# Kernel optimization log

Measured on AMD Instinct MI355X. Metric: run time of the kernel, lower is better.

Reference implementation:

```python
import jax, jax.numpy as jnp
import numpy as np

N = 50000      # nodes
E = 1200000    # edges (before self loops)
IN = 128       # in_channels
HID = 32       # hidden_channels
HEADS = 2
HC = HID * HEADS  # 64, per-layer output channels
OUT = 40       # classes
NEG_SLOPE = 0.2
BN_EPS = 1e-5


def setup_inputs() -> dict:
    key = jax.random.key(0)
    ks = jax.random.split(key, 20)
    def nrm(k, shape, scale=0.1):
        return jax.random.normal(k, shape, dtype=jnp.float32) * scale
    return {
        "x": jax.random.normal(ks[0], (N, IN), dtype=jnp.float32),
        "edge_index": jax.random.randint(ks[1], (2, E), 0, N),
        "W1": nrm(ks[2], (IN, HC)),
        "a_src1": nrm(ks[3], (HEADS, HID)),
        "a_dst1": nrm(ks[4], (HEADS, HID)),
        "b1": nrm(ks[5], (HC,)),
        "bn_gamma": 1.0 + nrm(ks[6], (HC,)),
        "bn_beta": nrm(ks[7], (HC,)),
        "bn_mean": nrm(ks[8], (HC,)),
        "bn_var": jax.random.uniform(ks[9], (HC,), minval=0.5, maxval=1.5),
        "W2": nrm(ks[10], (HC, HC)),
        "a_src2": nrm(ks[11], (HEADS, HID)),
        "a_dst2": nrm(ks[12], (HEADS, HID)),
        "b2": nrm(ks[13], (HC,)),
        "Wf": nrm(ks[14], (HC, OUT)),
        "bf": nrm(ks[15], (OUT,)),
    }


def _gat_conv(x, src, dst, W, a_s, a_d, b):
    # x: [N, F_in] -> h: [N, H, C]
    h = (x @ W).reshape(N, HEADS, HID)
    alpha_src = jnp.einsum("nhc,hc->nh", h, a_s)  # [N, H]
    alpha_dst = jnp.einsum("nhc,hc->nh", h, a_d)  # [N, H]
    e = alpha_src[src] + alpha_dst[dst]            # [E, H]
    e = jnp.where(e > 0, e, NEG_SLOPE * e)         # leaky_relu(0.2)
    # scatter softmax over edges grouped by dst node
    m = jax.ops.segment_max(e, dst, num_segments=N)
    m = jnp.where(jnp.isfinite(m), m, 0.0)         # isolated nodes -> -inf fill
    ee = jnp.exp(e - m[dst])
    denom = jax.ops.segment_sum(ee, dst, num_segments=N)
    alpha = ee / (denom[dst] + 1e-16)              # [E, H]
    # gather src features, weight by attention, scatter-add to dst
    out = jax.ops.segment_sum(h[src] * alpha[:, :, None], dst, num_segments=N)
    return out.reshape(N, HC) + b                  # concat heads + bias


def reference(x, edge_index, W1, a_src1, a_dst1, b1, bn_gamma, bn_beta,
              bn_mean, bn_var, W2, a_src2, a_dst2, b2, Wf, bf):
    # PyG GATConv adds self loops by default
    loop = jnp.arange(N, dtype=edge_index.dtype)
    src = jnp.concatenate([edge_index[0], loop])
    dst = jnp.concatenate([edge_index[1], loop])

    x1 = _gat_conv(x, src, dst, W1, a_src1, a_dst1, b1)
    x1 = (x1 - bn_mean) / jnp.sqrt(bn_var + BN_EPS) * bn_gamma + bn_beta  # BN eval
    x1 = jax.nn.elu(x1)
    # dropout is identity in eval mode
    x2 = _gat_conv(x1, src, dst, W2, a_src2, a_dst2, b2)
    jk = jnp.maximum(x1, x2)  # JumpingKnowledge 'max'
    logits = jk @ Wf + bf
    return jax.nn.log_softmax(logits, axis=1)
```

## Files before the change

kernel.cpp:

```cpp
#include <hip/hip_runtime.h>
#include <hip/hip_bf16.h>
#include <math.h>

#define N_NODES 50000
#define E_EDGES 1200000
#define E_TOT   (E_EDGES + N_NODES)
#define NEG_SLOPE 0.2f
#define BN_EPS 1e-5f
#define P_PART 196
#define B1 256
#define NSCAN (P_PART * B1)

__device__ __forceinline__ int rl_i(int v, int l) {
    return __builtin_amdgcn_readlane(v, l);
}
__device__ __forceinline__ float rl_f(float v, int l) {
    return __uint_as_float(__builtin_amdgcn_readlane(__float_as_uint(v), l));
}

__global__ void hist_kernel(const int* __restrict__ edst, unsigned* __restrict__ Ghist) {
    __shared__ unsigned hist[P_PART];
    for (int i = threadIdx.x; i < P_PART; i += 256) hist[i] = 0;
    __syncthreads();
    const int chunk = (E_TOT + B1 - 1) / B1;
    const int beg = blockIdx.x * chunk;
    const int end = min(beg + chunk, E_TOT);
    for (int i = beg + threadIdx.x; i < end; i += 256) {
        int d = (i < E_EDGES) ? edst[i] : (i - E_EDGES);
        atomicAdd(&hist[d >> 8], 1u);
    }
    __syncthreads();
    for (int p = threadIdx.x; p < P_PART; p += 256)
        Ghist[p * B1 + blockIdx.x] = hist[p];
}

__global__ void scan2_kernel(const unsigned* __restrict__ Ghist, unsigned* __restrict__ Goff) {
    __shared__ unsigned lds[1024];
    const int t = threadIdx.x;
    const int C = (NSCAN + 1023) / 1024;
    const int beg = t * C;
    const int end = min(beg + C, NSCAN);
    unsigned sum = 0;
    for (int i = beg; i < end; ++i) sum += Ghist[i];
    lds[t] = sum;
    __syncthreads();
    for (int off = 1; off < 1024; off <<= 1) {
        unsigned x = (t >= off) ? lds[t - off] : 0;
        __syncthreads();
        lds[t] += x;
        __syncthreads();
    }
    unsigned run = (t == 0) ? 0 : lds[t - 1];
    for (int i = beg; i < end; ++i) { Goff[i] = run; run += Ghist[i]; }
}

__global__ void partbase_kernel(const unsigned* __restrict__ Goff,
                                int* __restrict__ partbase, int* __restrict__ ptr) {
    int p = threadIdx.x;
    if (p < P_PART) partbase[p] = (int)Goff[p * B1];
    if (p == P_PART) partbase[P_PART] = E_TOT;
    if (p == 0) ptr[N_NODES] = E_TOT;
}

__global__ void scat2_kernel(const int* __restrict__ esrc, const int* __restrict__ edst,
                             const unsigned* __restrict__ Goff, unsigned* __restrict__ Gpart) {
    __shared__ unsigned cur[P_PART];
    for (int p = threadIdx.x; p < P_PART; p += 256) cur[p] = Goff[p * B1 + blockIdx.x];
    __syncthreads();
    const int chunk = (E_TOT + B1 - 1) / B1;
    const int beg = blockIdx.x * chunk;
    const int end = min(beg + chunk, E_TOT);
    for (int i = beg + threadIdx.x; i < end; i += 256) {
        int s = (i < E_EDGES) ? esrc[i] : (i - E_EDGES);
        int d = (i < E_EDGES) ? edst[i] : (i - E_EDGES);
        unsigned slot = atomicAdd(&cur[d >> 8], 1u);
        Gpart[slot] = ((unsigned)(d & 255) << 16) | (unsigned)s;
    }
}

__global__ void csr_kernel(const int* __restrict__ partbase, const unsigned* __restrict__ Gpart,
                           int* __restrict__ ptr, unsigned short* __restrict__ csr) {
    __shared__ unsigned deg[256];
    __shared__ unsigned scn[256];
    const int p = blockIdx.x;
    const int t = threadIdx.x;
    const int base = partbase[p];
    const int cnt = partbase[p + 1] - base;
    deg[t] = 0;
    __syncthreads();
    for (int i = t; i < cnt; i += 256)
        atomicAdd(&deg[Gpart[base + i] >> 16], 1u);
    __syncthreads();
    unsigned v = deg[t];
    scn[t] = v;
    __syncthreads();
    for (int o = 1; o < 256; o <<= 1) {
        unsigned x = (t >= o) ? scn[t - o] : 0;
        __syncthreads();
        scn[t] += x;
        __syncthreads();
    }
    unsigned excl = scn[t] - v;
    int node = p * 256 + t;
    if (node < N_NODES) ptr[node] = base + (int)excl;
    __syncthreads();
    deg[t] = excl;
    __syncthreads();
    for (int i = t; i < cnt; i += 256) {
        unsigned rec = Gpart[base + i];
        unsigned slot = atomicAdd(&deg[rec >> 16], 1u);
        csr[base + slot] = (unsigned short)(rec & 0xFFFFu);
    }
}

template<int K>
__global__ void lin_att_kernel(const float* __restrict__ x,
                               const float* __restrict__ W,
                               const float* __restrict__ a_s,
                               const float* __restrict__ a_d,
                               __hip_bfloat16* __restrict__ h,
                               float* __restrict__ asrc,
                               float* __restrict__ adst,
                               int n) {
    __shared__ float sW[K * 64];
    const int tid = threadIdx.x, lane = tid & 63;
    for (int i = tid; i < K * 64; i += 256) sW[i] = W[i];
    __syncthreads();
    const float a_sv = a_s[lane];
    const float a_dv = a_d[lane];
    const int wid = blockIdx.x * 4 + (tid >> 6);
    const int nwaves = gridDim.x * 4;
    for (int node = wid; node < n; node += nwaves) {
        float xr[K / 64];
        #pragma unroll
        for (int p = 0; p < K / 64; ++p) xr[p] = x[node * K + p * 64 + lane];
        float acc = 0.f;
        #pragma unroll
        for (int p = 0; p < K / 64; ++p) {
            #pragma unroll
            for (int k = 0; k < 64; ++k) {
                float xk = rl_f(xr[p], k);
                acc = fmaf(xk, sW[(p * 64 + k) * 64 + lane], acc);
            }
        }
        h[node * 64 + lane] = __float2bfloat16(acc);
        float ps = acc * a_sv, pd = acc * a_dv;
        #pragma unroll
        for (int m = 1; m < 32; m <<= 1) {
            ps += __shfl_xor(ps, m, 64);
            pd += __shfl_xor(pd, m, 64);
        }
        if ((lane & 31) == 0) {
            asrc[node * 2 + (lane >> 5)] = ps;
            adst[node * 2 + (lane >> 5)] = pd;
        }
    }
}

template<bool BN, bool FINAL>
__global__ void gat_agg_kernel(const int* __restrict__ ptr,
                               const unsigned short* __restrict__ csr_src,
                               const __hip_bfloat16* __restrict__ h,
                               const float2* __restrict__ asrc, const float2* __restrict__ adst,
                               const float* __restrict__ bias,
                               const float* __restrict__ gamma, const float* __restrict__ beta,
                               const float* __restrict__ mean, const float* __restrict__ var,
                               float* __restrict__ out,
                               const float* __restrict__ x1, const float* __restrict__ Wf,
                               const float* __restrict__ bf, float* __restrict__ out40) {
    __shared__ float sWf[FINAL ? 64 * 40 : 1];
    if constexpr (FINAL) {
        for (int i = threadIdx.x; i < 64 * 40; i += 256) sWf[i] = Wf[i];
        __syncthreads();
    }
    int node = blockIdx.x * 4 + (threadIdx.x >> 6);
    if (node >= N_NODES) return;
    const int lane = threadIdx.x & 63;
    const int half = lane & 31;
    float2 ad = adst[node];
    const float adh = (lane < 32) ? ad.x : ad.y;
    float m = -INFINITY, s = 0.f, acc = 0.f;
    const int beg = ptr[node], end = ptr[node + 1];
    for (int base = beg; base < end; base += 32) {
        const int cnt = min(32, end - base);
        int src = 0; float ev = -INFINITY;
        if (half < cnt) {
            src = (int)csr_src[base + half];
            float2 a2 = asrc[src];
            ev = ((lane < 32) ? a2.x : a2.y) + adh;
            ev = ev > 0.f ? ev : NEG_SLOPE * ev;
        }
        float cmax = ev;
        #pragma unroll
        for (int o = 1; o < 32; o <<= 1) cmax = fmaxf(cmax, __shfl_xor(cmax, o, 64));
        const float mn = fmaxf(m, cmax);
        const float rescale = __expf(m - mn);
        const float w = (half < cnt) ? __expf(ev - mn) : 0.f;
        float ws = w;
        #pragma unroll
        for (int o = 1; o < 32; o <<= 1) ws += __shfl_xor(ws, o, 64);
        s = s * rescale + ws;
        acc *= rescale;
        m = mn;
        int j = 0;
        for (; j + 4 <= cnt; j += 4) {
            int s0 = rl_i(src, j);
            int s1 = rl_i(src, j + 1);
            int s2 = rl_i(src, j + 2);
            int s3 = rl_i(src, j + 3);
            float wa0 = rl_f(w, j),      wb0 = rl_f(w, j + 32);
            float wa1 = rl_f(w, j + 1),  wb1 = rl_f(w, j + 33);
            float wa2 = rl_f(w, j + 2),  wb2 = rl_f(w, j + 34);
            float wa3 = rl_f(w, j + 3),  wb3 = rl_f(w, j + 35);
            float w0 = (lane < 32) ? wa0 : wb0;
            float w1 = (lane < 32) ? wa1 : wb1;
            float w2 = (lane < 32) ? wa2 : wb2;
            float w3 = (lane < 32) ? wa3 : wb3;
            float h0 = __bfloat162float(h[s0 * 64 + lane]);
            float h1 = __bfloat162float(h[s1 * 64 + lane]);
            float h2 = __bfloat162float(h[s2 * 64 + lane]);
            float h3 = __bfloat162float(h[s3 * 64 + lane]);
            acc = fmaf(w0, h0, acc);
            acc = fmaf(w1, h1, acc);
            acc = fmaf(w2, h2, acc);
            acc = fmaf(w3, h3, acc);
        }
        for (; j < cnt; ++j) {
            int sj = rl_i(src, j);
            float wa = rl_f(w, j), wb = rl_f(w, j + 32);
            float wj = (lane < 32) ? wa : wb;
            acc = fmaf(wj, __bfloat162float(h[sj * 64 + lane]), acc);
        }
    }
    float v = acc / (s + 1e-16f) + bias[lane];
    if constexpr (BN) {
        v = (v - mean[lane]) * rsqrtf(var[lane] + BN_EPS) * gamma[lane] + beta[lane];
        v = v > 0.f ? v : (__expf(v) - 1.f);
    }
    if constexpr (FINAL) {
        float jk = fmaxf(x1[node * 64 + lane], v);
        const int o = (lane < 40) ? lane : 0;
        float dot = 0.f;
        #pragma unroll
        for (int c = 0; c < 64; ++c) {
            float jv = rl_f(jk, c);
            dot = fmaf(jv, sWf[c * 40 + o], dot);
        }
        float logit = (lane < 40) ? (dot + bf[o]) : -INFINITY;
        float mx = logit;
        #pragma unroll
        for (int mm = 1; mm < 64; mm <<= 1) mx = fmaxf(mx, __shfl_xor(mx, mm, 64));
        float ex = (lane < 40) ? __expf(logit - mx) : 0.f;
        float sum = ex;
        #pragma unroll
        for (int mm = 1; mm < 64; mm <<= 1) sum += __shfl_xor(sum, mm, 64);
        if (lane < 40) out40[node * 40 + lane] = logit - mx - logf(sum);
    } else {
        out[node * 64 + lane] = v;
    }
}

extern "C" void kernel_launch(void* const* d_in, const int* in_sizes, int n_in,
                              void* d_out, int out_size, void* d_ws, size_t ws_size,
                              hipStream_t stream) {
    const float* x     = (const float*)d_in[0];
    const int*   ei    = (const int*)d_in[1];
    const float* W1    = (const float*)d_in[2];
    const float* as1   = (const float*)d_in[3];
    const float* ad1   = (const float*)d_in[4];
    const float* b1    = (const float*)d_in[5];
    const float* gamma = (const float*)d_in[6];
    const float* beta  = (const float*)d_in[7];
    const float* mean  = (const float*)d_in[8];
    const float* var   = (const float*)d_in[9];
    const float* W2    = (const float*)d_in[10];
    const float* as2   = (const float*)d_in[11];
    const float* ad2   = (const float*)d_in[12];
    const float* b2    = (const float*)d_in[13];
    const float* Wf    = (const float*)d_in[14];
    const float* bf    = (const float*)d_in[15];
    float* out = (float*)d_out;
    const int* esrc = ei;
    const int* edst = ei + E_EDGES;

    char* ws = (char*)d_ws;
    size_t off = 0;
    auto alloc = [&](size_t bytes) {
        char* p = ws + off;
        off += (bytes + 255) & ~(size_t)255;
        return p;
    };
    unsigned* Ghist = (unsigned*)alloc((size_t)NSCAN * 4);
    unsigned* Goff  = (unsigned*)alloc((size_t)NSCAN * 4);
    int* partbase   = (int*)alloc((size_t)(P_PART + 1) * 4);
    unsigned* Gpart = (unsigned*)alloc((size_t)E_TOT * 4);
    int* ptr             = (int*)alloc((size_t)(N_NODES + 1) * 4);
    unsigned short* csr  = (unsigned short*)alloc((size_t)E_TOT * 2);
    __hip_bfloat16* hbuf = (__hip_bfloat16*)alloc((size_t)N_NODES * 64 * 2);
    float* x1buf = (float*)alloc((size_t)N_NODES * 64 * 4);
    float* asrc  = (float*)alloc((size_t)N_NODES * 2 * 4);
    float* adst  = (float*)alloc((size_t)N_NODES * 2 * 4);
    (void)ws_size; (void)in_sizes; (void)n_in; (void)out_size;

    const int NB = (N_NODES + 3) / 4;

    hist_kernel<<<B1, 256, 0, stream>>>(edst, Ghist);
    scan2_kernel<<<1, 1024, 0, stream>>>(Ghist, Goff);
    partbase_kernel<<<1, 256, 0, stream>>>(Goff, partbase, ptr);
    scat2_kernel<<<B1, 256, 0, stream>>>(esrc, edst, Goff, Gpart);
    csr_kernel<<<P_PART, 256, 0, stream>>>(partbase, Gpart, ptr, csr);

    lin_att_kernel<128><<<2048, 256, 0, stream>>>(x, W1, as1, ad1, hbuf, asrc, adst, N_NODES);
    gat_agg_kernel<true, false><<<NB, 256, 0, stream>>>(ptr, csr, hbuf,
        (const float2*)asrc, (const float2*)adst,
        b1, gamma, beta, mean, var, x1buf, nullptr, nullptr, nullptr, nullptr);

    lin_att_kernel<64><<<2048, 256, 0, stream>>>(x1buf, W2, as2, ad2, hbuf, asrc, adst, N_NODES);
    gat_agg_kernel<false, true><<<NB, 256, 0, stream>>>(ptr, csr, hbuf,
        (const float2*)asrc, (const float2*)adst,
        b2, nullptr, nullptr, nullptr, nullptr, nullptr, x1buf, Wf, bf, out);
}
```

Baseline: 256.0 us.

## Precompute unnormalized edge attention weights and denominators in a separate per-partition kernel

```diff
diff --git a/kernel.cpp b/kernel.cpp
--- a/kernel.cpp
+++ b/kernel.cpp
@@ -16,6 +16,10 @@
 }
 __device__ __forceinline__ float rl_f(float v, int l) {
     return __uint_as_float(__builtin_amdgcn_readlane(__float_as_uint(v), l));
+}
+__device__ __forceinline__ unsigned bf16_bits(float f) {
+    unsigned u = __float_as_uint(f);
+    return (u + 0x7FFFu + ((u >> 16) & 1u)) >> 16;
 }
 
 __global__ void hist_kernel(const int* __restrict__ edst, unsigned* __restrict__ Ghist) {
@@ -79,7 +83,8 @@
 }
 
 __global__ void csr_kernel(const int* __restrict__ partbase, const unsigned* __restrict__ Gpart,
-                           int* __restrict__ ptr, unsigned short* __restrict__ csr) {
+                           int* __restrict__ ptr, unsigned short* __restrict__ csr,
+                           unsigned short* __restrict__ dl16) {
     __shared__ unsigned deg[256];
     __shared__ unsigned scn[256];
     const int p = blockIdx.x;
@@ -108,8 +113,47 @@
     __syncthreads();
     for (int i = t; i < cnt; i += 256) {
         unsigned rec = Gpart[base + i];
-        unsigned slot = atomicAdd(&deg[rec >> 16], 1u);
-        csr[base + slot] = (unsigned short)(rec & 0xFFFFu);
+        unsigned dl = rec >> 16;
+        unsigned slot = atomicAdd(&deg[dl], 1u);
+        csr[base + slot]  = (unsigned short)(rec & 0xFFFFu);
+        dl16[base + slot] = (unsigned short)dl;
+    }
+}
+
+__global__ void ew_kernel(const int* __restrict__ partbase,
+                          const unsigned short* __restrict__ csr,
+                          const unsigned short* __restrict__ dl16,
+                          const float2* __restrict__ asrc,
+                          const float2* __restrict__ adst,
+                          uint2* __restrict__ wrec,
+                          float2* __restrict__ denom) {
+    __shared__ float2 sad[256];
+    __shared__ float sden[512];
+    const int p = blockIdx.x, t = threadIdx.x;
+    if (t < 256) {
+        int node = p * 256 + t;
+        sad[t] = (node < N_NODES) ? adst[node] : make_float2(0.f, 0.f);
+    }
+    if (t < 512) sden[t] = 0.f;
+    __syncthreads();
+    const int base = partbase[p];
+    const int cnt = partbase[p + 1] - base;
+    for (int i = t; i < cnt; i += 1024) {
+        int s  = (int)csr[base + i];
+        int dl = (int)dl16[base + i];
+        float2 a = asrc[s];
+        float2 b = sad[dl];
+        float e0 = a.x + b.x; e0 = e0 > 0.f ? e0 : NEG_SLOPE * e0;
+        float e1 = a.y + b.y; e1 = e1 > 0.f ? e1 : NEG_SLOPE * e1;
+        float w0 = __expf(e0), w1 = __expf(e1);
+        atomicAdd(&sden[dl * 2 + 0], w0);
+        atomicAdd(&sden[dl * 2 + 1], w1);
+        wrec[base + i] = make_uint2((unsigned)s | (bf16_bits(w0) << 16), bf16_bits(w1));
+    }
+    __syncthreads();
+    if (t < 256) {
+        int node = p * 256 + t;
+        if (node < N_NODES) denom[node] = make_float2(sden[t * 2], sden[t * 2 + 1]);
     }
 }
 
@@ -159,9 +203,9 @@
 
 template<bool BN, bool FINAL>
 __global__ void gat_agg_kernel(const int* __restrict__ ptr,
-                               const unsigned short* __restrict__ csr_src,
+                               const uint2* __restrict__ wrec,
+                               const float2* __restrict__ denom,
                                const __hip_bfloat16* __restrict__ h,
-                               const float2* __restrict__ asrc, const float2* __restrict__ adst,
                                const float* __restrict__ bias,
                                const float* __restrict__ gamma, const float* __restrict__ beta,
                                const float* __restrict__ mean, const float* __restrict__ var,
@@ -177,62 +221,33 @@
     if (node >= N_NODES) return;
     const int lane = threadIdx.x & 63;
     const int half = lane & 31;
-    float2 ad = adst[node];
-    const float adh = (lane < 32) ? ad.x : ad.y;
-    float m = -INFINITY, s = 0.f, acc = 0.f;
+    const bool lo = (lane < 32);
+    float2 dn = denom[node];
+    const float den = lo ? dn.x : dn.y;
+    float acc = 0.f;
     const int beg = ptr[node], end = ptr[node + 1];
+
+#define EDGE(J) {                                                            \
+        unsigned rx = (unsigned)rl_i((int)rec.x, (J));                       \
+        unsigned ry = (unsigned)rl_i((int)rec.y, (J));                       \
+        const __hip_bfloat16* hp = h + (size_t)(rx & 0xFFFFu) * 64u;         \
+        float wv = __uint_as_float(lo ? (rx & 0xFFFF0000u) : (ry << 16));    \
+        acc = fmaf(wv, __bfloat162float(hp[lane]), acc); }
+
     for (int base = beg; base < end; base += 32) {
         const int cnt = min(32, end - base);
-        int src = 0; float ev = -INFINITY;
-        if (half < cnt) {
-            src = (int)csr_src[base + half];
-            float2 a2 = asrc[src];
-            ev = ((lane < 32) ? a2.x : a2.y) + adh;
-            ev = ev > 0.f ? ev : NEG_SLOPE * ev;
-        }
-        float cmax = ev;
-        #pragma unroll
-        for (int o = 1; o < 32; o <<= 1) cmax = fmaxf(cmax, __shfl_xor(cmax, o, 64));
-        const float mn = fmaxf(m, cmax);
-        const float rescale = __expf(m - mn);
-        const float w = (half < cnt) ? __expf(ev - mn) : 0.f;
-        float ws = w;
-        #pragma unroll
-        for (int o = 1; o < 32; o <<= 1) ws += __shfl_xor(ws, o, 64);
-        s = s * rescale + ws;
-        acc *= rescale;
-        m = mn;
+        uint2 rec = make_uint2(0u, 0u);
+        if (half < cnt) rec = wrec[base + half];
         int j = 0;
-        for (; j + 4 <= cnt; j += 4) {
-            int s0 = rl_i(src, j);
-            int s1 = rl_i(src, j + 1);
-            int s2 = rl_i(src, j + 2);
-            int s3 = rl_i(src, j + 3);
-            float wa0 = rl_f(w, j),      wb0 = rl_f(w, j + 32);
-            float wa1 = rl_f(w, j + 1),  wb1 = rl_f(w, j + 33);
-            float wa2 = rl_f(w, j + 2),  wb2 = rl_f(w, j + 34);
-            float wa3 = rl_f(w, j + 3),  wb3 = rl_f(w, j + 35);
-            float w0 = (lane < 32) ? wa0 : wb0;
-            float w1 = (lane < 32) ? wa1 : wb1;
-            float w2 = (lane < 32) ? wa2 : wb2;
-            float w3 = (lane < 32) ? wa3 : wb3;
-            float h0 = __bfloat162float(h[s0 * 64 + lane]);
-            float h1 = __bfloat162float(h[s1 * 64 + lane]);
-            float h2 = __bfloat162float(h[s2 * 64 + lane]);
-            float h3 = __bfloat162float(h[s3 * 64 + lane]);
-            acc = fmaf(w0, h0, acc);
-            acc = fmaf(w1, h1, acc);
-            acc = fmaf(w2, h2, acc);
-            acc = fmaf(w3, h3, acc);
-        }
-        for (; j < cnt; ++j) {
-            int sj = rl_i(src, j);
-            float wa = rl_f(w, j), wb = rl_f(w, j + 32);
-            float wj = (lane < 32) ? wa : wb;
-            acc = fmaf(wj, __bfloat162float(h[sj * 64 + lane]), acc);
-        }
-    }
-    float v = acc / (s + 1e-16f) + bias[lane];
+        for (; j + 8 <= cnt; j += 8) {
+            EDGE(j) EDGE(j + 1) EDGE(j + 2) EDGE(j + 3)
+            EDGE(j + 4) EDGE(j + 5) EDGE(j + 6) EDGE(j + 7)
+        }
+        for (; j < cnt; ++j) { EDGE(j) }
+    }
+#undef EDGE
+
+    float v = acc / (den + 1e-16f) + bias[lane];
     if constexpr (BN) {
         v = (v - mean[lane]) * rsqrtf(var[lane] + BN_EPS) * gamma[lane] + beta[lane];
         v = v > 0.f ? v : (__expf(v) - 1.f);
@@ -294,9 +309,12 @@
     unsigned* Goff  = (unsigned*)alloc((size_t)NSCAN * 4);
     int* partbase   = (int*)alloc((size_t)(P_PART + 1) * 4);
     unsigned* Gpart = (unsigned*)alloc((size_t)E_TOT * 4);
-    int* ptr             = (int*)alloc((size_t)(N_NODES + 1) * 4);
-    unsigned short* csr  = (unsigned short*)alloc((size_t)E_TOT * 2);
-    __hip_bfloat16* hbuf = (__hip_bfloat16*)alloc((size_t)N_NODES * 64 * 2);
+    int* ptr              = (int*)alloc((size_t)(N_NODES + 1) * 4);
+    unsigned short* csr   = (unsigned short*)alloc((size_t)E_TOT * 2);
+    unsigned short* dl16  = (unsigned short*)alloc((size_t)E_TOT * 2);
+    uint2* wrec           = (uint2*)alloc((size_t)E_TOT * 8);
+    float2* denom         = (float2*)alloc((size_t)N_NODES * 8);
+    __hip_bfloat16* hbuf  = (__hip_bfloat16*)alloc((size_t)N_NODES * 64 * 2);
     float* x1buf = (float*)alloc((size_t)N_NODES * 64 * 4);
     float* asrc  = (float*)alloc((size_t)N_NODES * 2 * 4);
     float* adst  = (float*)alloc((size_t)N_NODES * 2 * 4);
@@ -308,15 +326,17 @@
     scan2_kernel<<<1, 1024, 0, stream>>>(Ghist, Goff);
     partbase_kernel<<<1, 256, 0, stream>>>(Goff, partbase, ptr);
     scat2_kernel<<<B1, 256, 0, stream>>>(esrc, edst, Goff, Gpart);
-    csr_kernel<<<P_PART, 256, 0, stream>>>(partbase, Gpart, ptr, csr);
+    csr_kernel<<<P_PART, 256, 0, stream>>>(partbase, Gpart, ptr, csr, dl16);
 
     lin_att_kernel<128><<<2048, 256, 0, stream>>>(x, W1, as1, ad1, hbuf, asrc, adst, N_NODES);
-    gat_agg_kernel<true, false><<<NB, 256, 0, stream>>>(ptr, csr, hbuf,
-        (const float2*)asrc, (const float2*)adst,
+    ew_kernel<<<P_PART, 1024, 0, stream>>>(partbase, csr, dl16,
+        (const float2*)asrc, (const float2*)adst, wrec, denom);
+    gat_agg_kernel<true, false><<<NB, 256, 0, stream>>>(ptr, wrec, denom, hbuf,
         b1, gamma, beta, mean, var, x1buf, nullptr, nullptr, nullptr, nullptr);
 
     lin_att_kernel<64><<<2048, 256, 0, stream>>>(x1buf, W2, as2, ad2, hbuf, asrc, adst, N_NODES);
-    gat_agg_kernel<false, true><<<NB, 256, 0, stream>>>(ptr, csr, hbuf,
-        (const float2*)asrc, (const float2*)adst,
+    ew_kernel<<<P_PART, 1024, 0, stream>>>(partbase, csr, dl16,
+        (const float2*)asrc, (const float2*)adst, wrec, denom);
+    gat_agg_kernel<false, true><<<NB, 256, 0, stream>>>(ptr, wrec, denom, hbuf,
         b2, nullptr, nullptr, nullptr, nullptr, nullptr, x1buf, Wf, bf, out);
 }
```

Result: slower. 290.5 us (+13.5%).
